# Performance work log

Measured on AMD Instinct MI355X. Metric: run time of the kernel, lower is better.

Reference implementation:

```python
import jax, jax.numpy as jnp
import numpy as np

# Involution2D config (matches init_kwargs)
F = 256          # filters
K = 3            # kernel_size
G = 16           # groups
RR = 4           # reduce_ratio
BN_EPS = 1e-3    # keras BatchNormalization default epsilon


def setup_inputs() -> dict:
    key = jax.random.key(0)
    ks = jax.random.split(key, 8)
    C = 256
    Cr = F // RR                    # reduce_mapping channels = 64
    KKG = K * K * G                 # span_mapping channels = 144
    s = lambda k, sh, fan: jax.random.normal(k, sh, jnp.float32) * (1.0 / np.sqrt(fan))
    return {
        "x": jax.random.normal(ks[0], (4, 128, 128, C), jnp.float32),
        # reduce_mapping: 1x1 conv + BN(inference) + relu
        "Wr": s(ks[1], (C, Cr), C),
        "br": jnp.zeros((Cr,), jnp.float32),
        "gamma": jnp.ones((Cr,), jnp.float32),
        "beta": jnp.zeros((Cr,), jnp.float32),
        "mean": jax.random.normal(ks[2], (Cr,), jnp.float32) * 0.1,
        "var": jax.random.uniform(ks[3], (Cr,), jnp.float32, 0.5, 1.5),
        # span_mapping: 1x1 conv -> K*K*G dynamic weights
        "Ws": s(ks[4], (Cr, KKG), Cr),
        "bs": jnp.zeros((KKG,), jnp.float32),
        # initial_mapping: 1x1 conv -> F (applied since F != K*K*G)
        "Wi": s(ks[5], (C, F), C),
        "bi": jnp.zeros((F,), jnp.float32),
    }


def reference(x, Wr, br, gamma, beta, mean, var, Ws, bs, Wi, bi):
    B, H, W, _ = x.shape
    KK = K * K
    # reduce_mapping: 1x1 conv + BN(inference) + relu
    r = jnp.einsum('bhwc,cd->bhwd', x, Wr) + br
    r = jax.nn.relu((r - mean) * jax.lax.rsqrt(var + BN_EPS) * gamma + beta)
    # span_mapping: per-pixel dynamic kernel weights [B,H,W,KK*G] -> [B,H,W,G,1,KK]
    w = jnp.einsum('bhwd,dk->bhwk', r, Ws) + bs
    w = w.reshape(B, H, W, G, KK)[:, :, :, :, None, :]
    # initial_mapping: 1x1 conv -> F channels
    xi = jnp.einsum('bhwc,cf->bhwf', x, Wi) + bi
    # tf.image.extract_patches (SAME, stride=1, rate=1): layout is
    # (kernel_pos major, channel minor), i.e. flat index = kpos*F + c
    pad = (K - 1) // 2
    xp = jnp.pad(xi, ((0, 0), (pad, pad), (pad, pad), (0, 0)))
    patches = jnp.stack(
        [xp[:, i:i + H, j:j + W, :] for i in range(K) for j in range(K)],
        axis=3)                                   # [B,H,W,KK,F]
    # faithful to the original K.reshape of the flat [KK*F] axis
    patches = patches.reshape(B, H, W, G, F // G, KK)
    out = jnp.sum(w * patches, axis=-1)           # [B,H,W,G,F//G]
    return out.reshape(B, H, W, F)
```

## Files before the change

### kernel.cpp

```cpp
#include <hip/hip_runtime.h>

#define BN_EPS 1e-3f

typedef __attribute__((ext_vector_type(8))) short bf16x8;
typedef __attribute__((ext_vector_type(4))) float f32x4;

__device__ inline unsigned short f2b(float f) {
    unsigned int u = __float_as_uint(f);
    unsigned int r = (u + 0x7fffu + ((u >> 16) & 1u)) >> 16;
    return (unsigned short)r;
}
__device__ inline float b2f(unsigned short h) {
    return __uint_as_float(((unsigned int)h) << 16);
}

__global__ void k_prep(const float* __restrict__ Wi, const float* __restrict__ Wr,
                       const float* __restrict__ Ws,
                       unsigned short* __restrict__ Bt, unsigned short* __restrict__ Wst) {
    int t = blockIdx.x * 256 + threadIdx.x;
    if (t < 320 * 256) {
        int n = t >> 8, k = t & 255;
        float v = (n < 256) ? Wi[k * 256 + n] : Wr[k * 64 + (n - 256)];
        Bt[t] = f2b(v);
    } else {
        int t2 = t - 320 * 256;
        if (t2 < 144 * 64) {
            int n = t2 >> 6, k = t2 & 63;
            Wst[t2] = f2b(Ws[k * 144 + n]);
        }
    }
}

#define XIP 264
#define RS_OFF (180 * XIP)
#define RSP 72
#define WL_OFF (RS_OFF + 180 * RSP)
#define SMN (WL_OFF + 128 * 144)

__global__ __launch_bounds__(1024, 4) void k_fused(
    const float* __restrict__ x, const unsigned short* __restrict__ Bt,
    const unsigned short* __restrict__ Wst,
    const float* __restrict__ bi, const float* __restrict__ br,
    const float* __restrict__ gamma, const float* __restrict__ beta,
    const float* __restrict__ mean, const float* __restrict__ var,
    const float* __restrict__ bs, float* __restrict__ out)
{
    __shared__ __attribute__((aligned(16))) unsigned short sm[SMN];
    const int tid = threadIdx.x;
    const int bx = blockIdx.x;
    const int w0 = (bx & 7) * 16;
    const int h0 = ((bx >> 3) & 15) * 8;
    const int bb = bx >> 7;

    const int wv = tid >> 6;
    const int lane = tid & 63;
    const int col = lane & 15;
    const int quad = lane >> 4;

    const float bi_v = bi[wv * 16 + col];
    const int dcl = (wv & 3) * 16 + col;
    const float brd = br[dcl];
    const float md  = mean[dcl];
    const float sc  = gamma[dcl] * rsqrtf(var[dcl] + BN_EPS);
    const float btv = beta[dcl];

    bf16x8 bxA[8], brr[8];
    {
        const unsigned short* p0 = &Bt[(wv * 16 + col) * 256];
#pragma unroll
        for (int kc = 0; kc < 8; ++kc)
            bxA[kc] = *(const bf16x8*)&p0[kc * 32 + quad * 8];
        if (wv < 4) {
            const unsigned short* pr = &Bt[((16 + wv) * 16 + col) * 256];
#pragma unroll
            for (int kc = 0; kc < 8; ++kc)
                brr[kc] = *(const bf16x8*)&pr[kc * 32 + quad * 8];
        }
    }

    const int chq = (tid & 31) * 4;

    {
        int hp = tid >> 5;
        int r = hp / 18, cc = hp - r * 18;
        int gh = h0 - 1 + r, gw = w0 - 1 + cc;
        bool ok = ((unsigned)gh < 128u) && ((unsigned)gw < 128u);
        float4 v0, v1;
        if (ok) {
            const float* src = x + (((long long)(bb * 128 + gh)) * 128 + gw) * 256 + chq;
            v0 = *(const float4*)&src[0];
            v1 = *(const float4*)&src[128];
        } else {
            v0 = (float4){0.f, 0.f, 0.f, 0.f};
            v1 = v0;
        }
        uint2 pk;
        pk.x = (unsigned)f2b(v0.x) | ((unsigned)f2b(v0.y) << 16);
        pk.y = (unsigned)f2b(v0.z) | ((unsigned)f2b(v0.w) << 16);
        *(uint2*)&sm[hp * XIP + chq] = pk;
        pk.x = (unsigned)f2b(v1.x) | ((unsigned)f2b(v1.y) << 16);
        pk.y = (unsigned)f2b(v1.z) | ((unsigned)f2b(v1.w) << 16);
        *(uint2*)&sm[hp * XIP + chq + 128] = pk;
    }
    __syncthreads();

    for (int c = 0; c < 6; ++c) {
        float4 vn0, vn1;
        int hp_n = 192;
        if (c < 5) {
            hp_n = (c + 1) * 32 + (tid >> 5);
            int r = hp_n / 18, cc = hp_n - r * 18;
            int gh = h0 - 1 + r, gw = w0 - 1 + cc;
            bool ok = (hp_n < 180) && ((unsigned)gh < 128u) && ((unsigned)gw < 128u);
            if (ok) {
                const float* src = x + (((long long)(bb * 128 + gh)) * 128 + gw) * 256 + chq;
                vn0 = *(const float4*)&src[0];
                vn1 = *(const float4*)&src[128];
            } else {
                vn0 = (float4){0.f, 0.f, 0.f, 0.f};
                vn1 = vn0;
            }
        }

        f32x4 acc0 = {0.f, 0.f, 0.f, 0.f}, acc1 = acc0;
        f32x4 ar0 = acc0, ar1 = acc0;
        {
            const int rowA0 = (c * 32 + col) * XIP;
            const int rowA1 = rowA0 + 16 * XIP;
#pragma unroll
            for (int kc = 0; kc < 8; ++kc) {
                const int kb = kc * 32 + quad * 8;
                bf16x8 a0 = *(const bf16x8*)&sm[rowA0 + kb];
                bf16x8 a1 = *(const bf16x8*)&sm[rowA1 + kb];
                acc0 = __builtin_amdgcn_mfma_f32_16x16x32_bf16(a0, bxA[kc], acc0, 0, 0, 0);
                acc1 = __builtin_amdgcn_mfma_f32_16x16x32_bf16(a1, bxA[kc], acc1, 0, 0, 0);
                if (wv < 4) {
                    ar0 = __builtin_amdgcn_mfma_f32_16x16x32_bf16(a0, brr[kc], ar0, 0, 0, 0);
                    ar1 = __builtin_amdgcn_mfma_f32_16x16x32_bf16(a1, brr[kc], ar1, 0, 0, 0);
                }
            }
        }
        __syncthreads();

        if (c < 5 && hp_n < 180) {
            uint2 pk;
            pk.x = (unsigned)f2b(vn0.x) | ((unsigned)f2b(vn0.y) << 16);
            pk.y = (unsigned)f2b(vn0.z) | ((unsigned)f2b(vn0.w) << 16);
            *(uint2*)&sm[hp_n * XIP + chq] = pk;
            pk.x = (unsigned)f2b(vn1.x) | ((unsigned)f2b(vn1.y) << 16);
            pk.y = (unsigned)f2b(vn1.z) | ((unsigned)f2b(vn1.w) << 16);
            *(uint2*)&sm[hp_n * XIP + chq + 128] = pk;
        }

        {
            const int n0 = wv * 16 + col;
            const int rb = c * 32 + quad * 4;
#pragma unroll
            for (int rg = 0; rg < 4; ++rg) {
                const int r0 = rb + rg, r1 = r0 + 16;
                if (r0 < 180) sm[r0 * XIP + n0] = f2b(acc0[rg] + bi_v);
                if (r1 < 180) sm[r1 * XIP + n0] = f2b(acc1[rg] + bi_v);
            }
            if (wv < 4) {
#pragma unroll
                for (int rg = 0; rg < 4; ++rg) {
                    const int r0 = rb + rg, r1 = r0 + 16;
                    if (r0 < 180) {
                        float v = (ar0[rg] + brd - md) * sc + btv;
                        sm[RS_OFF + r0 * RSP + dcl] = f2b(fmaxf(v, 0.f));
                    }
                    if (r1 < 180) {
                        float v = (ar1[rg] + brd - md) * sc + btv;
                        sm[RS_OFF + r1 * RSP + dcl] = f2b(fmaxf(v, 0.f));
                    }
                }
            }
        }
        __syncthreads();
    }

    {
        const int m = wv & 7;
        const int jbase = (wv >> 3) * 4;
        f32x4 wacc[5];
#pragma unroll
        for (int jj = 0; jj < 5; ++jj) wacc[jj] = (f32x4){0.f, 0.f, 0.f, 0.f};
        const int arow = (19 + m * 18 + col) * RSP;
#pragma unroll
        for (int kc = 0; kc < 2; ++kc) {
            const int kb = kc * 32 + quad * 8;
            bf16x8 ra = *(const bf16x8*)&sm[RS_OFF + arow + kb];
#pragma unroll
            for (int jj = 0; jj < 5; ++jj) {
                bf16x8 wb = *(const bf16x8*)&Wst[((jbase + jj) * 16 + col) * 64 + kb];
                wacc[jj] = __builtin_amdgcn_mfma_f32_16x16x32_bf16(ra, wb, wacc[jj], 0, 0, 0);
            }
        }
#pragma unroll
        for (int jj = 0; jj < 5; ++jj) {
            const int n = (jbase + jj) * 16 + col;
            const float bv = bs[n];
            const int prow = m * 16 + quad * 4;
#pragma unroll
            for (int rg = 0; rg < 4; ++rg)
                sm[WL_OFF + (prow + rg) * 144 + n] = f2b(wacc[jj][rg] + bv);
        }
    }
    __syncthreads();

    {
        const int g = tid & 15;
        const int pb = tid >> 4;

        const int idx0 = g * 144;
        const int kp0  = idx0 >> 8;
        const int c0   = idx0 & 255;
        int len1 = 256 - c0; if (len1 > 144) len1 = 144;
        const int kp1  = kp0 + 1;
        const int koff0 = (kp0 / 3) * 18 + (kp0 % 3);
        const int koff1 = (kp1 <= 8) ? ((kp1 / 3) * 18 + (kp1 % 3)) : 0;

#pragma unroll
        for (int jj = 0; jj < 2; ++jj) {
            const int p = pb + 64 * jj;
            const int phb = (p >> 4) * 18 + (p & 15);
            const int base0 = (phb + koff0) * XIP + c0;
            const int base1 = (phb + koff1) * XIP;

            float wf[9];
#pragma unroll
            for (int kk = 0; kk < 9; ++kk)
                wf[kk] = b2f(sm[WL_OFF + p * 144 + g * 9 + kk]);

            float res[16];
            {
                int4 xv[9];
#pragma unroll
                for (int i = 0; i < 9; ++i) {
                    const int e = i * 8;
                    const int addr = (e < len1) ? (base0 + e) : (base1 + (e - len1));
                    xv[i] = *(const int4*)&sm[addr];
                }
#pragma unroll
                for (int f2 = 0; f2 < 8; ++f2) {
                    float a = 0.f;
#pragma unroll
                    for (int kk = 0; kk < 9; ++kk) {
                        const int e = f2 * 9 + kk;
                        const int word = ((const int*)&xv[e >> 3])[(e >> 1) & 3];
                        const unsigned short u = (e & 1) ? (unsigned short)(((unsigned)word) >> 16)
                                                         : (unsigned short)(word & 0xffff);
                        a += wf[kk] * b2f(u);
                    }
                    res[f2] = a;
                }
            }
            {
                int4 xv[9];
#pragma unroll
                for (int i = 9; i < 18; ++i) {
                    const int e = i * 8;
                    const int addr = (e < len1) ? (base0 + e) : (base1 + (e - len1));
                    xv[i - 9] = *(const int4*)&sm[addr];
                }
#pragma unroll
                for (int f2 = 8; f2 < 16; ++f2) {
                    float a = 0.f;
#pragma unroll
                    for (int kk = 0; kk < 9; ++kk) {
                        const int e = f2 * 9 + kk;
                        const int i = (e >> 3) - 9;
                        const int word = ((const int*)&xv[i])[(e >> 1) & 3];
                        const unsigned short u = (e & 1) ? (unsigned short)(((unsigned)word) >> 16)
                                                         : (unsigned short)(word & 0xffff);
                        a += wf[kk] * b2f(u);
                    }
                    res[f2] = a;
                }
            }

            const long long orow =
                (((long long)(bb * 128 + h0 + (p >> 4))) * 128 + (w0 + (p & 15))) * 256 + g * 16;
#pragma unroll
            for (int q = 0; q < 4; ++q) {
                float4 o = {res[q * 4 + 0], res[q * 4 + 1], res[q * 4 + 2], res[q * 4 + 3]};
                *(float4*)&out[orow + q * 4] = o;
            }
        }
    }
}

extern "C" void kernel_launch(void* const* d_in, const int* in_sizes, int n_in,
                              void* d_out, int out_size, void* d_ws, size_t ws_size,
                              hipStream_t stream) {
    const float* x     = (const float*)d_in[0];
    const float* Wr    = (const float*)d_in[1];
    const float* br    = (const float*)d_in[2];
    const float* gamma = (const float*)d_in[3];
    const float* beta  = (const float*)d_in[4];
    const float* mean  = (const float*)d_in[5];
    const float* var   = (const float*)d_in[6];
    const float* Ws    = (const float*)d_in[7];
    const float* bs    = (const float*)d_in[8];
    const float* Wi    = (const float*)d_in[9];
    const float* bi    = (const float*)d_in[10];
    float* out = (float*)d_out;

    unsigned char* ws = (unsigned char*)d_ws;
    unsigned short* Bt  = (unsigned short*)(ws + 0);
    unsigned short* Wst = (unsigned short*)(ws + 163840);

    k_prep<<<dim3(356), dim3(256), 0, stream>>>(Wi, Wr, Ws, Bt, Wst);
    k_fused<<<dim3(512), dim3(1024), 0, stream>>>(
        x, Bt, Wst, bi, br, gamma, beta, mean, var, bs, out);
}
```

Before: 179.1 us.

## Shrink spatial tile to 8x8 with 512-thread blocks and alias weight LDS

Changes the per-block tile from 8x16 pixels to 8x8, halving threads per block to 512 and doubling the grid. Each wave now computes two 16-column output slices of the initial mapping per row chunk, and the dynamic-weight buffer reuses the reduce-mapping LDS region after a barrier. The aim is to cut LDS per block so more blocks fit per CU and occupancy rises. In exchange, the halo overhead grows (100 halo pixels for 64 outputs instead of 180 for 128), so more x is reloaded and more redundant 1x1 conv work is done.

```diff
diff --git a/kernel.cpp b/kernel.cpp
--- a/kernel.cpp
+++ b/kernel.cpp
@@ -32,12 +32,13 @@
 }
 
 #define XIP 264
-#define RS_OFF (180 * XIP)
+#define NHROW 100
+#define RS_OFF (NHROW * XIP)
 #define RSP 72
-#define WL_OFF (RS_OFF + 180 * RSP)
-#define SMN (WL_OFF + 128 * 144)
-
-__global__ __launch_bounds__(1024, 4) void k_fused(
+#define WL_OFF RS_OFF
+#define SMN (RS_OFF + 64 * 144)
+
+__global__ __launch_bounds__(512, 4) void k_fused(
     const float* __restrict__ x, const unsigned short* __restrict__ Bt,
     const unsigned short* __restrict__ Wst,
     const float* __restrict__ bi, const float* __restrict__ br,
@@ -48,30 +49,32 @@
     __shared__ __attribute__((aligned(16))) unsigned short sm[SMN];
     const int tid = threadIdx.x;
     const int bx = blockIdx.x;
-    const int w0 = (bx & 7) * 16;
-    const int h0 = ((bx >> 3) & 15) * 8;
-    const int bb = bx >> 7;
+    const int w0 = (bx & 15) * 8;
+    const int h0 = ((bx >> 4) & 15) * 8;
+    const int bb = bx >> 8;
 
     const int wv = tid >> 6;
     const int lane = tid & 63;
     const int col = lane & 15;
     const int quad = lane >> 4;
 
-    const float bi_v = bi[wv * 16 + col];
+    const float bi_v0 = bi[wv * 16 + col];
+    const float bi_v1 = bi[(wv + 8) * 16 + col];
     const int dcl = (wv & 3) * 16 + col;
-    const float brd = br[dcl];
-    const float md  = mean[dcl];
-    const float sc  = gamma[dcl] * rsqrtf(var[dcl] + BN_EPS);
-    const float btv = beta[dcl];
-
-    bf16x8 bxA[8], brr[8];
+    const float r_sc = gamma[dcl] * rsqrtf(var[dcl] + BN_EPS);
+    const float r_bias = (br[dcl] - mean[dcl]) * r_sc + beta[dcl];
+
+    bf16x8 bx0[8], bx1[8], brr[8];
     {
         const unsigned short* p0 = &Bt[(wv * 16 + col) * 256];
-#pragma unroll
-        for (int kc = 0; kc < 8; ++kc)
-            bxA[kc] = *(const bf16x8*)&p0[kc * 32 + quad * 8];
+        const unsigned short* p1 = &Bt[((wv + 8) * 16 + col) * 256];
+#pragma unroll
+        for (int kc = 0; kc < 8; ++kc) {
+            bx0[kc] = *(const bf16x8*)&p0[kc * 32 + quad * 8];
+            bx1[kc] = *(const bf16x8*)&p1[kc * 32 + quad * 8];
+        }
         if (wv < 4) {
-            const unsigned short* pr = &Bt[((16 + wv) * 16 + col) * 256];
+            const unsigned short* pr = &Bt[(256 + wv * 16 + col) * 256];
 #pragma unroll
             for (int kc = 0; kc < 8; ++kc)
                 brr[kc] = *(const bf16x8*)&pr[kc * 32 + quad * 8];
@@ -79,12 +82,13 @@
     }
 
     const int chq = (tid & 31) * 4;
+    const int hpt = tid >> 5;
 
     {
-        int hp = tid >> 5;
-        int r = hp / 18, cc = hp - r * 18;
-        int gh = h0 - 1 + r, gw = w0 - 1 + cc;
-        bool ok = ((unsigned)gh < 128u) && ((unsigned)gw < 128u);
+        const int hp = hpt;
+        const int hr = hp / 10, hc = hp - hr * 10;
+        const int gh = h0 - 1 + hr, gw = w0 - 1 + hc;
+        const bool ok = ((unsigned)gh < 128u) && ((unsigned)gw < 128u);
         float4 v0, v1;
         if (ok) {
             const float* src = x + (((long long)(bb * 128 + gh)) * 128 + gw) * 256 + chq;
@@ -104,14 +108,14 @@
     }
     __syncthreads();
 
-    for (int c = 0; c < 6; ++c) {
+    for (int c = 0; c < 7; ++c) {
         float4 vn0, vn1;
-        int hp_n = 192;
-        if (c < 5) {
-            hp_n = (c + 1) * 32 + (tid >> 5);
-            int r = hp_n / 18, cc = hp_n - r * 18;
-            int gh = h0 - 1 + r, gw = w0 - 1 + cc;
-            bool ok = (hp_n < 180) && ((unsigned)gh < 128u) && ((unsigned)gw < 128u);
+        int hp_n = 200;
+        if (c < 6) {
+            hp_n = (c + 1) * 16 + hpt;
+            const int hr = hp_n / 10, hc = hp_n - hr * 10;
+            const int gh = h0 - 1 + hr, gw = w0 - 1 + hc;
+            const bool ok = (hp_n < NHROW) && ((unsigned)gh < 128u) && ((unsigned)gw < 128u);
             if (ok) {
                 const float* src = x + (((long long)(bb * 128 + gh)) * 128 + gw) * 256 + chq;
                 vn0 = *(const float4*)&src[0];
@@ -122,27 +126,22 @@
             }
         }
 
-        f32x4 acc0 = {0.f, 0.f, 0.f, 0.f}, acc1 = acc0;
-        f32x4 ar0 = acc0, ar1 = acc0;
+        f32x4 acc0 = {0.f, 0.f, 0.f, 0.f}, acc1 = acc0, ar = acc0;
         {
-            const int rowA0 = (c * 32 + col) * XIP;
-            const int rowA1 = rowA0 + 16 * XIP;
+            const int rowA = (c * 16 + col) * XIP;
 #pragma unroll
             for (int kc = 0; kc < 8; ++kc) {
                 const int kb = kc * 32 + quad * 8;
-                bf16x8 a0 = *(const bf16x8*)&sm[rowA0 + kb];
-                bf16x8 a1 = *(const bf16x8*)&sm[rowA1 + kb];
-                acc0 = __builtin_amdgcn_mfma_f32_16x16x32_bf16(a0, bxA[kc], acc0, 0, 0, 0);
-                acc1 = __builtin_amdgcn_mfma_f32_16x16x32_bf16(a1, bxA[kc], acc1, 0, 0, 0);
-                if (wv < 4) {
-                    ar0 = __builtin_amdgcn_mfma_f32_16x16x32_bf16(a0, brr[kc], ar0, 0, 0, 0);
-                    ar1 = __builtin_amdgcn_mfma_f32_16x16x32_bf16(a1, brr[kc], ar1, 0, 0, 0);
-                }
+                bf16x8 a0 = *(const bf16x8*)&sm[rowA + kb];
+                acc0 = __builtin_amdgcn_mfma_f32_16x16x32_bf16(a0, bx0[kc], acc0, 0, 0, 0);
+                acc1 = __builtin_amdgcn_mfma_f32_16x16x32_bf16(a0, bx1[kc], acc1, 0, 0, 0);
+                if (wv < 4)
+                    ar = __builtin_amdgcn_mfma_f32_16x16x32_bf16(a0, brr[kc], ar, 0, 0, 0);
             }
         }
         __syncthreads();
 
-        if (c < 5 && hp_n < 180) {
+        if (c < 6 && hp_n < NHROW) {
             uint2 pk;
             pk.x = (unsigned)f2b(vn0.x) | ((unsigned)f2b(vn0.y) << 16);
             pk.y = (unsigned)f2b(vn0.z) | ((unsigned)f2b(vn0.w) << 16);
@@ -154,25 +153,23 @@
 
         {
             const int n0 = wv * 16 + col;
-            const int rb = c * 32 + quad * 4;
+            const int rb = c * 16 + quad * 4;
 #pragma unroll
             for (int rg = 0; rg < 4; ++rg) {
-                const int r0 = rb + rg, r1 = r0 + 16;
-                if (r0 < 180) sm[r0 * XIP + n0] = f2b(acc0[rg] + bi_v);
-                if (r1 < 180) sm[r1 * XIP + n0] = f2b(acc1[rg] + bi_v);
+                const int r0 = rb + rg;
+                if (r0 < NHROW) {
+                    sm[r0 * XIP + n0] = f2b(acc0[rg] + bi_v0);
+                    sm[r0 * XIP + n0 + 128] = f2b(acc1[rg] + bi_v1);
+                }
             }
             if (wv < 4) {
 #pragma unroll
                 for (int rg = 0; rg < 4; ++rg) {
-                    const int r0 = rb + rg, r1 = r0 + 16;
-                    if (r0 < 180) {
-                        float v = (ar0[rg] + brd - md) * sc + btv;
+                    const int r0 = rb + rg;
+                    if (r0 < NHROW) {
+                        float v = ar[rg] * r_sc + r_bias;
                         sm[RS_OFF + r0 * RSP + dcl] = f2b(fmaxf(v, 0.f));
                     }
-                    if (r1 < 180) {
-                        float v = (ar1[rg] + brd - md) * sc + btv;
-                        sm[RS_OFF + r1 * RSP + dcl] = f2b(fmaxf(v, 0.f));
-                    }
                 }
             }
         }
@@ -180,50 +177,59 @@
     }
 
     {
-        const int m = wv & 7;
-        const int jbase = (wv >> 3) * 4;
+        const int m = wv & 3;
+        const int jh = wv >> 2;
+        const int jb = jh * 5;
+        const int njt = 5 - jh;
+        const int p2 = m * 16 + col;
+        const int arow = RS_OFF + (((p2 >> 3) + 1) * 10 + (p2 & 7) + 1) * RSP;
+        bf16x8 ra0 = *(const bf16x8*)&sm[arow + quad * 8];
+        bf16x8 ra1 = *(const bf16x8*)&sm[arow + 32 + quad * 8];
+        __syncthreads();
+
         f32x4 wacc[5];
 #pragma unroll
         for (int jj = 0; jj < 5; ++jj) wacc[jj] = (f32x4){0.f, 0.f, 0.f, 0.f};
-        const int arow = (19 + m * 18 + col) * RSP;
-#pragma unroll
-        for (int kc = 0; kc < 2; ++kc) {
-            const int kb = kc * 32 + quad * 8;
-            bf16x8 ra = *(const bf16x8*)&sm[RS_OFF + arow + kb];
-#pragma unroll
-            for (int jj = 0; jj < 5; ++jj) {
-                bf16x8 wb = *(const bf16x8*)&Wst[((jbase + jj) * 16 + col) * 64 + kb];
-                wacc[jj] = __builtin_amdgcn_mfma_f32_16x16x32_bf16(ra, wb, wacc[jj], 0, 0, 0);
-            }
-        }
 #pragma unroll
         for (int jj = 0; jj < 5; ++jj) {
-            const int n = (jbase + jj) * 16 + col;
-            const float bv = bs[n];
-            const int prow = m * 16 + quad * 4;
-#pragma unroll
-            for (int rg = 0; rg < 4; ++rg)
-                sm[WL_OFF + (prow + rg) * 144 + n] = f2b(wacc[jj][rg] + bv);
+            if (jj < njt) {
+                const unsigned short* wp = &Wst[((jb + jj) * 16 + col) * 64];
+                bf16x8 wb0 = *(const bf16x8*)&wp[quad * 8];
+                bf16x8 wb1 = *(const bf16x8*)&wp[32 + quad * 8];
+                wacc[jj] = __builtin_amdgcn_mfma_f32_16x16x32_bf16(ra0, wb0, wacc[jj], 0, 0, 0);
+                wacc[jj] = __builtin_amdgcn_mfma_f32_16x16x32_bf16(ra1, wb1, wacc[jj], 0, 0, 0);
+            }
+        }
+#pragma unroll
+        for (int jj = 0; jj < 5; ++jj) {
+            if (jj < njt) {
+                const int n = (jb + jj) * 16 + col;
+                const float bv = bs[n];
+                const int prow = m * 16 + quad * 4;
+#pragma unroll
+                for (int rg = 0; rg < 4; ++rg)
+                    sm[WL_OFF + (prow + rg) * 144 + n] = f2b(wacc[jj][rg] + bv);
+            }
         }
     }
     __syncthreads();
 
     {
-        const int g = tid & 15;
-        const int pb = tid >> 4;
+        const int g = tid >> 5;
+        const int pidx = tid & 31;
 
         const int idx0 = g * 144;
         const int kp0  = idx0 >> 8;
         const int c0   = idx0 & 255;
         int len1 = 256 - c0; if (len1 > 144) len1 = 144;
         const int kp1  = kp0 + 1;
-        const int koff0 = (kp0 / 3) * 18 + (kp0 % 3);
-        const int koff1 = (kp1 <= 8) ? ((kp1 / 3) * 18 + (kp1 % 3)) : 0;
+        const int koff0 = (kp0 / 3) * 10 + (kp0 % 3);
+        const int koff1 = (kp1 <= 8) ? ((kp1 / 3) * 10 + (kp1 % 3)) : 0;
 
 #pragma unroll
         for (int jj = 0; jj < 2; ++jj) {
-            const int p = pb + 64 * jj;
-            const int phb = (p >> 4) * 18 + (p & 15);
+            const int p = pidx + 32 * jj;
+            const int phb = (p >> 3) * 10 + (p & 7);
             const int base0 = (phb + koff0) * XIP + c0;
             const int base1 = (phb + koff1) * XIP;
 
@@ -280,7 +286,7 @@
             }
 
             const long long orow =
-                (((long long)(bb * 128 + h0 + (p >> 4))) * 128 + (w0 + (p & 15))) * 256 + g * 16;
+                (((long long)(bb * 128 + h0 + (p >> 3))) * 128 + (w0 + (p & 7))) * 256 + g * 16;
 #pragma unroll
             for (int q = 0; q < 4; ++q) {
                 float4 o = {res[q * 4 + 0], res[q * 4 + 1], res[q * 4 + 2], res[q * 4 + 3]};
@@ -311,6 +317,6 @@
     unsigned short* Wst = (unsigned short*)(ws + 163840);
 
     k_prep<<<dim3(356), dim3(256), 0, stream>>>(Wi, Wr, Ws, Bt, Wst);
-    k_fused<<<dim3(512), dim3(1024), 0, stream>>>(
+    k_fused<<<dim3(1024), dim3(512), 0, stream>>>(
         x, Bt, Wst, bi, br, gamma, beta, mean, var, bs, out);
 }
```

New measurement: 203.9 us. +13.8%, slower.
